# Kernel tuning notes

Hardware: AMD Instinct MI355X
Metric: run time of the kernel (lower is better)

The kernel has to match this reference:

```python
import jax, jax.numpy as jnp
import numpy as np

NUM_SLOTS = 8
SLOT_DIM = 3
WRITE_RATE = 0.1


def _amu(x, memory, Wk, bk, Ww, bw, Wg, bg, Wo, bo):
    """Associative Memory Unit.
    x: [B, T, Din], memory: [B, N, D] -> (outputs [B, T, Dout], memory [B, N, D]).
    Per step: softmax key-addressing read, gated erase/add write at WRITE_RATE,
    output = Linear(concat(x_t, read)).
    """
    xt = jnp.swapaxes(x, 0, 1)  # [T, B, Din]

    def step(mem, x_t):
        k = x_t @ Wk + bk                                   # [B, D]
        scores = jnp.einsum('bnd,bd->bn', mem, k)           # [B, N]
        w = jax.nn.softmax(scores, axis=-1)                 # addressing weights
        read = jnp.einsum('bn,bnd->bd', w, mem)             # [B, D]
        v = x_t @ Ww + bw                                   # write vector [B, D]
        e = jax.nn.sigmoid(x_t @ Wg + bg)                   # erase gate [B, D]
        we = w[:, :, None] * e[:, None, :]                  # [B, N, D]
        mem = mem * (1.0 - WRITE_RATE * we) + WRITE_RATE * w[:, :, None] * v[:, None, :]
        out = jnp.concatenate([x_t, read], axis=-1) @ Wo + bo
        return mem, out

    mem, outs = jax.lax.scan(step, memory, xt)
    return jnp.swapaxes(outs, 0, 1), mem


def setup_inputs() -> dict:
    key = jax.random.key(0)
    ks = jax.random.split(key, 12)
    B, T, D_in, D_hid, D_out = 64, 512, 128, 512, 128
    s = 0.05
    return {
        'inp': jax.random.normal(ks[0], (B, T, D_in), jnp.float32),
        'W1k': jax.random.normal(ks[1], (D_in, SLOT_DIM), jnp.float32) * s,
        'b1k': jnp.zeros((SLOT_DIM,), jnp.float32),
        'W1w': jax.random.normal(ks[2], (D_in, SLOT_DIM), jnp.float32) * s,
        'b1w': jnp.zeros((SLOT_DIM,), jnp.float32),
        'W1g': jax.random.normal(ks[3], (D_in, SLOT_DIM), jnp.float32) * s,
        'b1g': jnp.zeros((SLOT_DIM,), jnp.float32),
        'W1o': jax.random.normal(ks[4], (D_in + SLOT_DIM, D_hid), jnp.float32) * s,
        'b1o': jnp.zeros((D_hid,), jnp.float32),
        'W2k': jax.random.normal(ks[5], (D_hid, SLOT_DIM), jnp.float32) * s,
        'b2k': jnp.zeros((SLOT_DIM,), jnp.float32),
        'W2w': jax.random.normal(ks[6], (D_hid, SLOT_DIM), jnp.float32) * s,
        'b2w': jnp.zeros((SLOT_DIM,), jnp.float32),
        'W2g': jax.random.normal(ks[7], (D_hid, SLOT_DIM), jnp.float32) * s,
        'b2g': jnp.zeros((SLOT_DIM,), jnp.float32),
        'W2o': jax.random.normal(ks[8], (D_hid + SLOT_DIM, D_out), jnp.float32) * s,
        'b2o': jnp.zeros((D_out,), jnp.float32),
    }


def reference(inp, W1k, b1k, W1w, b1w, W1g, b1g, W1o, b1o,
              W2k, b2k, W2w, b2w, W2g, b2g, W2o, b2o):
    B = inp.shape[0]
    mem0 = jnp.zeros((B, NUM_SLOTS, SLOT_DIM), inp.dtype)
    o1, mem = _amu(inp, mem0, W1k, b1k, W1w, b1w, W1g, b1g, W1o, b1o)
    o1 = jax.nn.sigmoid(o1)  # self.layers = Sequential(Sigmoid())
    o2, mem = _amu(o1, mem, W2k, b2k, W2w, b2w, W2g, b2g, W2o, b2o)
    out = jax.nn.sigmoid(o2[:, -1, :])  # last timestep, then sigmoid
    return out
```

## Files before the change

kernel.cpp:

```cpp
#include <hip/hip_runtime.h>
#include <hip/hip_bf16.h>

#define B_ 64
#define T_ 512
#define LOG2E 1.4426950408889634f
#define PHASE_STEPS 16
#define NPHASE (T_/PHASE_STEPS)

typedef __attribute__((ext_vector_type(8))) short short8;
typedef __attribute__((ext_vector_type(4))) float f32x4;

__device__ __forceinline__ float fast_exp2(float x){ return __builtin_amdgcn_exp2f(x); }
__device__ __forceinline__ float fast_rcp(float x){ return __builtin_amdgcn_rcpf(x); }
__device__ __forceinline__ float sigmoidf_(float x){ return fast_rcp(1.0f + fast_exp2(-x*LOG2E)); }
__device__ __forceinline__ unsigned short f2bf(float f){
  union{float f; unsigned u;} v; v.f = f;
  unsigned r = v.u + 0x7fffu + ((v.u>>16)&1u);
  return (unsigned short)(r>>16);
}
__device__ __forceinline__ float bf2f(unsigned short u){
  union{unsigned u; float f;} v; v.u = ((unsigned)u)<<16; return v.f;
}

template<int CTRL>
__device__ __forceinline__ float dpp_xadd(float x){
  int y = __builtin_amdgcn_update_dpp(0, __float_as_int(x), CTRL, 0xf, 0xf, true);
  return x + __int_as_float(y);
}
__device__ __forceinline__ float dpp_sum8(float x){
  x = dpp_xadd<0xB1>(x);
  x = dpp_xadd<0x4E>(x);
  x = dpp_xadd<0x141>(x);
  return x;
}

__device__ __forceinline__ void lds_barrier(){
  asm volatile("s_waitcnt lgkmcnt(0)" ::: "memory");
  __builtin_amdgcn_s_barrier();
  asm volatile("" ::: "memory");
}

__global__ __launch_bounds__(256) void k_proj1(const float* __restrict__ X,
    const float* __restrict__ Wk, const float* __restrict__ bk,
    const float* __restrict__ Ww, const float* __restrict__ bw,
    const float* __restrict__ Wg, const float* __restrict__ bg,
    float* __restrict__ P1,
    const float* __restrict__ W1o,
    const float* __restrict__ W2k, const float* __restrict__ W2w, const float* __restrict__ W2g,
    unsigned short* __restrict__ W1oTb, unsigned short* __restrict__ W2cTb)
{
  __shared__ __align__(16) float A[64*132];
  __shared__ __align__(16) float WcT[9*132];
  __shared__ float bb[9];
  int tid = threadIdx.x;
  if (blockIdx.x >= 512){
    int idx = ((int)blockIdx.x - 512)*256 + tid;
    if (idx < 65536){
      int n = idx >> 7, k = idx & 127;
      W1oTb[idx] = f2bf(W1o[k*512 + n]);
    }
    if (idx < 8192){
      int j = idx >> 9, c = idx & 511;
      float v = 0.f;
      if (j < 3) v = W2k[c*3 + j];
      else if (j < 6) v = W2w[c*3 + j - 3];
      else if (j < 9) v = W2g[c*3 + j - 6];
      W2cTb[idx] = f2bf(v);
    }
    return;
  }
  long r0 = (long)blockIdx.x * 64;
  const float4* X4 = (const float4*)(X + r0*128);
  #pragma unroll
  for (int it=0; it<8; ++it){
    int f4 = tid + it*256;
    float4 v = X4[f4];
    int f = f4*4; int row = f>>7; int k = f&127;
    *(float4*)&A[row*132+k] = v;
  }
  #pragma unroll
  for (int it=0; it<5; ++it){
    int w0 = tid + it*256;
    if (w0 < 1152){
      int k = w0/9, j = w0%9;
      float val;
      if (j<3) val = Wk[k*3+j]; else if (j<6) val = Ww[k*3+j-3]; else val = Wg[k*3+j-6];
      WcT[j*132+k] = val;
    }
  }
  if (tid < 9){
    float v; if (tid<3) v = bk[tid]; else if (tid<6) v = bw[tid-3]; else v = bg[tid-6];
    bb[tid] = v;
  }
  __syncthreads();
  for (int o = tid; o < 576; o += 256){
    int row = o/9, j = o%9;
    const f32x4* Ar = (const f32x4*)(A + row*132);
    const f32x4* Wr = (const f32x4*)(WcT + j*132);
    f32x4 acc4 = {0.f,0.f,0.f,0.f};
    #pragma unroll
    for (int k4=0;k4<32;++k4){
      f32x4 a = Ar[k4], wv = Wr[k4];
      acc4[0]=fmaf(a[0],wv[0],acc4[0]);
      acc4[1]=fmaf(a[1],wv[1],acc4[1]);
      acc4[2]=fmaf(a[2],wv[2],acc4[2]);
      acc4[3]=fmaf(a[3],wv[3],acc4[3]);
    }
    float acc = bb[j] + (acc4[0]+acc4[1]) + (acc4[2]+acc4[3]);
    if (j<3) acc *= LOG2E;
    else if (j<6) acc *= 0.1f;
    else acc = 0.1f * sigmoidf_(acc);
    long r = r0 + row;
    int b = (int)(r >> 9); int t = (int)(r & 511);
    int bh = b >> 5, bl = b & 31;
    P1[(((long)bh*512 + t)*32 + bl)*12 + j] = acc;
  }
}

template<int STORE_SM>
__device__ __forceinline__ void scan_slim(const float* __restrict__ P,
                                          float* __restrict__ Out, int bh)
{
  __shared__ __align__(16) float buf[2][PHASE_STEPS*32*12];
  int tid = threadIdx.x;
  int wv = tid >> 6, lane = tid & 63;
  const float* Pb = P + (long)bh*512*384;
  if (wv == 8){
    #pragma unroll 1
    for (int p = 0; p < NPHASE; ++p){
      const float4* s4 = (const float4*)Pb + (long)p*1536;
      float4* d4 = (float4*)buf[p&1];
      #pragma unroll
      for (int c=0;c<2;++c){
        float4 tmp[12];
        #pragma unroll
        for (int i=0;i<12;++i) tmp[i] = s4[lane + (c*12+i)*64];
        #pragma unroll
        for (int i=0;i<12;++i) d4[lane + (c*12+i)*64] = tmp[i];
      }
      lds_barrier();
    }
    return;
  }
  if (lane >= 32) return;
  int g = lane >> 3, slot = lane & 7;
  int bl = wv*4 + g;
  int batch = bh*32 + bl;
  float* So = Out + ((long)batch*8 + slot)*4;
  float m0=0.f, m1=0.f, m2=0.f;
  f32x4 pfa[4], pfb[4]; float pfc[4];
  lds_barrier();
  #pragma unroll 1
  for (int p = 0; p < NPHASE; ++p){
    const float* bp = buf[p&1] + bl*12;
    const f32x4* bp4 = (const f32x4*)bp;
    #pragma unroll
    for (int u=0;u<3;++u){
      pfa[u]=bp4[u*96]; pfb[u]=bp4[u*96+1]; pfc[u]=bp[u*384+8];
    }
    #pragma unroll
    for (int s=0;s<PHASE_STEPS;++s){
      f32x4 A0=pfa[s&3], A1=pfb[s&3]; float e2=pfc[s&3];
      if (s+3 < PHASE_STEPS){
        int i3=(s+3)&3;
        pfa[i3]=bp4[(s+3)*96]; pfb[i3]=bp4[(s+3)*96+1]; pfc[i3]=bp[(s+3)*384+8];
      }
      float sc = fmaf(m2, A0[2], fmaf(m1, A0[1], m0*A0[0]));
      float pe = fast_exp2(sc);
      float S = dpp_sum8(pe);
      float rinv = fast_rcp(S);
      float w = pe * rinv;
      if (STORE_SM){
        f32x4 sv; sv[0]=pe; sv[1]=m0; sv[2]=m1; sv[3]=m2;
        *(f32x4*)(So + (long)(p*PHASE_STEPS+s)*2048) = sv;
      } else if (p == NPHASE-1 && s == PHASE_STEPS-1){
        float r0 = dpp_sum8(pe*m0);
        float r1 = dpp_sum8(pe*m1);
        float r2 = dpp_sum8(pe*m2);
        float rsel = (slot==0) ? r0 : ((slot==1) ? r1 : r2);
        rsel *= rinv;
        if (slot < 3) Out[slot*64 + batch] = rsel;
      }
      float v0=A0[3], v1=A1[0], v2=A1[1], e0=A1[2], e1=A1[3];
      m0 = fmaf(w, fmaf(-e0, m0, v0), m0);
      m1 = fmaf(w, fmaf(-e1, m1, v1), m1);
      m2 = fmaf(w, fmaf(-e2, m2, v2), m2);
    }
    if (p < NPHASE-1) lds_barrier();
  }
}

__global__ __launch_bounds__(576) void k_scan1(const float* __restrict__ P1,
                                               float* __restrict__ SM)
{
  scan_slim<1>(P1, SM, (int)blockIdx.x);
}

__global__ __launch_bounds__(576) void k_mega1(const float* __restrict__ P1,
    float* __restrict__ SM, const float* __restrict__ X,
    const unsigned short* __restrict__ W1oTb, const float* __restrict__ b1o,
    unsigned short* __restrict__ z1bf)
{
  if (blockIdx.x < 2){
    scan_slim<1>(P1, SM, (int)blockIdx.x);
    return;
  }
  int tid = threadIdx.x;
  if (tid >= 512) return;
  int w8 = tid >> 6, lane = tid & 63;
  int n16 = lane & 15, g4 = lane >> 4;
  long r0 = (long)(blockIdx.x - 2) * 16;

  short8 afr[4];
  const float* Xrow = X + (r0 + n16)*128;
  #pragma unroll
  for (int q=0;q<4;++q){
    f32x4 x0 = *(const f32x4*)(Xrow + q*32 + g4*8);
    f32x4 x1 = *(const f32x4*)(Xrow + q*32 + g4*8 + 4);
    short8 a;
    a[0]=(short)f2bf(x0[0]); a[1]=(short)f2bf(x0[1]);
    a[2]=(short)f2bf(x0[2]); a[3]=(short)f2bf(x0[3]);
    a[4]=(short)f2bf(x1[0]); a[5]=(short)f2bf(x1[1]);
    a[6]=(short)f2bf(x1[2]); a[7]=(short)f2bf(x1[3]);
    afr[q]=a;
  }
  #pragma unroll
  for (int tt=0; tt<4; ++tt){
    int gc = w8*64 + tt*16 + n16;
    f32x4 acc = {0.f,0.f,0.f,0.f};
    #pragma unroll
    for (int q=0;q<4;++q){
      short8 bf = *(const short8*)(W1oTb + gc*128 + q*32 + g4*8);
      acc = __builtin_amdgcn_mfma_f32_16x16x32_bf16(afr[q], bf, acc, 0,0,0);
    }
    float bias = b1o[gc];
    #pragma unroll
    for (int reg=0; reg<4; ++reg){
      int rowloc = g4*4 + reg;
      z1bf[(r0 + rowloc)*512 + gc] = f2bf(acc[reg] + bias);
    }
  }
}

__global__ __launch_bounds__(256) void k_fused2(
    const unsigned short* __restrict__ z1bf, const float* __restrict__ W1o,
    const float* __restrict__ SM, const unsigned short* __restrict__ W2cTb,
    const float* __restrict__ b2k, const float* __restrict__ b2w, const float* __restrict__ b2g,
    float* __restrict__ P2, float* __restrict__ O1last)
{
  __shared__ __align__(16) float rdS[48];
  __shared__ __align__(16) unsigned short o1b[16*520];
  __shared__ __align__(16) float pSum[4*16*16];
  int tid = threadIdx.x;
  long r0 = (long)blockIdx.x * 16;
  int b = (int)(r0 >> 9); int t0 = (int)(r0 & 511);

  if (tid < 128){
    int i = tid >> 3, slot = tid & 7;
    f32x4 v = *(const f32x4*)(SM + (((long)(t0+i)*64 + b)*8 + slot)*4);
    float S   = dpp_sum8(v[0]);
    float r0v = dpp_sum8(v[0]*v[1]);
    float r1v = dpp_sum8(v[0]*v[2]);
    float r2v = dpp_sum8(v[0]*v[3]);
    float rinv = fast_rcp(S);
    float rsel = (slot==0) ? r0v : ((slot==1) ? r1v : r2v);
    if (slot < 3) rdS[i*3+slot] = rsel*rinv;
  }
  __syncthreads();

  {
    int row = tid >> 4, seg = tid & 15, c0 = seg*32;
    float rd0v = rdS[row*3+0], rd1v = rdS[row*3+1], rd2v = rdS[row*3+2];
    const unsigned short* zr = z1bf + (r0 + row)*512 + c0;
    bool last = (t0 == 496) && (row == 15);
    #pragma unroll
    for (int ch=0; ch<4; ++ch){
      short8 z8 = *(const short8*)(zr + ch*8);
      int cc = c0 + ch*8;
      f32x4 wa0 = *(const f32x4*)(W1o + 128*512 + cc);
      f32x4 wa1 = *(const f32x4*)(W1o + 128*512 + cc + 4);
      f32x4 wb0 = *(const f32x4*)(W1o + 129*512 + cc);
      f32x4 wb1 = *(const f32x4*)(W1o + 129*512 + cc + 4);
      f32x4 wc0 = *(const f32x4*)(W1o + 130*512 + cc);
      f32x4 wc1 = *(const f32x4*)(W1o + 130*512 + cc + 4);
      #pragma unroll
      for (int j=0;j<8;++j){
        float z = bf2f((unsigned short)z8[j]);
        float w0 = (j<4)? wa0[j&3] : wa1[j&3];
        float w1 = (j<4)? wb0[j&3] : wb1[j&3];
        float w2 = (j<4)? wc0[j&3] : wc1[j&3];
        float o1 = sigmoidf_(z + rd0v*w0 + rd1v*w1 + rd2v*w2);
        o1b[row*520 + cc + j] = f2bf(o1);
        if (last) O1last[b*512 + cc + j] = o1;
      }
    }
  }
  __syncthreads();

  int w = tid >> 6, lane = tid & 63;
  int n16 = lane & 15, g4 = lane >> 4;
  f32x4 accP = {0.f,0.f,0.f,0.f};
  #pragma unroll
  for (int q2=0; q2<4; ++q2){
    int kk = w*128 + q2*32;
    short8 a2 = *(const short8*)(o1b + n16*520 + kk + g4*8);
    short8 bb2 = *(const short8*)(W2cTb + n16*512 + kk + g4*8);
    accP = __builtin_amdgcn_mfma_f32_16x16x32_bf16(a2, bb2, accP, 0,0,0);
  }
  #pragma unroll
  for (int reg=0;reg<4;++reg){
    int rowloc = g4*4+reg;
    pSum[w*256 + rowloc*16 + n16] = accP[reg];
  }
  __syncthreads();
  if (tid < 144){
    int r = tid/9, j = tid%9;
    float s = pSum[r*16+j] + pSum[256+r*16+j] + pSum[512+r*16+j] + pSum[768+r*16+j];
    float outv;
    if (j<3){ s += b2k[j]; outv = s*LOG2E; }
    else if (j<6){ s += b2w[j-3]; outv = 0.1f*s; }
    else { s += b2g[j-6]; outv = 0.1f*sigmoidf_(s); }
    int t = t0 + r;
    int bh = b >> 5, bl = b & 31;
    P2[(((long)bh*512 + t)*32 + bl)*12 + j] = outv;
  }
}

__global__ __launch_bounds__(256) void k_fused(const float* __restrict__ X,
    const float* __restrict__ W1o, const float* __restrict__ b1o,
    const float* __restrict__ SM,
    const unsigned short* __restrict__ W1oTb, const unsigned short* __restrict__ W2cTb,
    const float* __restrict__ b2k, const float* __restrict__ b2w, const float* __restrict__ b2g,
    float* __restrict__ P2, float* __restrict__ O1last)
{
  __shared__ __align__(16) float rdS[48];
  __shared__ __align__(16) unsigned short o1b[16*520];
  __shared__ __align__(16) float pSum[4*16*16];
  int tid = threadIdx.x;
  int w = tid >> 6, lane = tid & 63;
  int n16 = lane & 15, g4 = lane >> 4;
  long r0 = (long)blockIdx.x * 16;
  int b = (int)(r0 >> 9); int t0 = (int)(r0 & 511);

  if (tid < 128){
    int i = tid >> 3, slot = tid & 7;
    f32x4 v = *(const f32x4*)(SM + (((long)(t0+i)*64 + b)*8 + slot)*4);
    float S   = dpp_sum8(v[0]);
    float r0v = dpp_sum8(v[0]*v[1]);
    float r1v = dpp_sum8(v[0]*v[2]);
    float r2v = dpp_sum8(v[0]*v[3]);
    float rinv = fast_rcp(S);
    float rsel = (slot==0) ? r0v : ((slot==1) ? r1v : r2v);
    if (slot < 3) rdS[i*3+slot] = rsel*rinv;
  }

  short8 afr[4];
  const float* Xrow = X + (r0 + n16)*128;
  #pragma unroll
  for (int q=0;q<4;++q){
    f32x4 x0 = *(const f32x4*)(Xrow + q*32 + g4*8);
    f32x4 x1 = *(const f32x4*)(Xrow + q*32 + g4*8 + 4);
    short8 a;
    a[0]=(short)f2bf(x0[0]); a[1]=(short)f2bf(x0[1]);
    a[2]=(short)f2bf(x0[2]); a[3]=(short)f2bf(x0[3]);
    a[4]=(short)f2bf(x1[0]); a[5]=(short)f2bf(x1[1]);
    a[6]=(short)f2bf(x1[2]); a[7]=(short)f2bf(x1[3]);
    afr[q]=a;
  }
  __syncthreads();

  f32x4 ra = *(const f32x4*)(rdS + g4*12);
  f32x4 rb = *(const f32x4*)(rdS + g4*12 + 4);
  f32x4 rc = *(const f32x4*)(rdS + g4*12 + 8);
  float rd0[4] = { ra[0], ra[3], rb[2], rc[1] };
  float rd1[4] = { ra[1], rb[0], rb[3], rc[2] };
  float rd2[4] = { ra[2], rb[1], rc[0], rc[3] };

  #pragma unroll
  for (int tt=0; tt<8; ++tt){
    int gc = w*128 + tt*16 + n16;
    f32x4 acc = {0.f,0.f,0.f,0.f};
    #pragma unroll
    for (int q=0;q<4;++q){
      short8 bf = *(const short8*)(W1oTb + gc*128 + q*32 + g4*8);
      acc = __builtin_amdgcn_mfma_f32_16x16x32_bf16(afr[q], bf, acc, 0,0,0);
    }
    float bias = b1o[gc];
    float wr0 = W1o[128*512+gc], wr1 = W1o[129*512+gc], wr2 = W1o[130*512+gc];
    #pragma unroll
    for (int reg=0; reg<4; ++reg){
      int rowloc = g4*4 + reg;
      float z = acc[reg] + bias + rd0[reg]*wr0 + rd1[reg]*wr1 + rd2[reg]*wr2;
      float o1 = sigmoidf_(z);
      o1b[rowloc*520 + gc] = f2bf(o1);
      if (t0 == 496 && rowloc == 15) O1last[b*512 + gc] = o1;
    }
  }

  f32x4 accP = {0.f,0.f,0.f,0.f};
  #pragma unroll
  for (int q2=0; q2<4; ++q2){
    int kk = w*128 + q2*32;
    short8 a2 = *(const short8*)(o1b + n16*520 + kk + g4*8);
    short8 bb2 = *(const short8*)(W2cTb + n16*512 + kk + g4*8);
    accP = __builtin_amdgcn_mfma_f32_16x16x32_bf16(a2, bb2, accP, 0,0,0);
  }
  #pragma unroll
  for (int reg=0;reg<4;++reg){
    int rowloc = g4*4+reg;
    pSum[w*256 + rowloc*16 + n16] = accP[reg];
  }
  __syncthreads();
  if (tid < 144){
    int r = tid/9, j = tid%9;
    float s = pSum[r*16+j] + pSum[256+r*16+j] + pSum[512+r*16+j] + pSum[768+r*16+j];
    float outv;
    if (j<3){ s += b2k[j]; outv = s*LOG2E; }
    else if (j<6){ s += b2w[j-3]; outv = 0.1f*s; }
    else { s += b2g[j-6]; outv = 0.1f*sigmoidf_(s); }
    int t = t0 + r;
    int bh = b >> 5, bl = b & 31;
    P2[(((long)bh*512 + t)*32 + bl)*12 + j] = outv;
  }
}

__global__ __launch_bounds__(576) void k_scan2_opart(const float* __restrict__ P2,
    float* __restrict__ R2F,
    const float* __restrict__ O1last, const float* __restrict__ W2o,
    const float* __restrict__ b2o, float* __restrict__ Opart)
{
  if (blockIdx.x < 2){
    scan_slim<0>(P2, R2F, (int)blockIdx.x);
    return;
  }
  __shared__ __align__(16) float s2[512];
  int b = blockIdx.x - 2; int tid = threadIdx.x;
  if (tid < 128)
    ((float4*)s2)[tid] = ((const float4*)(O1last + b*512))[tid];
  __syncthreads();
  if (tid < 128){
    float acc = b2o[tid];
    #pragma unroll 8
    for (int n=0;n<512;++n) acc = fmaf(s2[n], W2o[n*128+tid], acc);
    Opart[b*128+tid] = acc;
  }
}

__global__ __launch_bounds__(256) void k_final(const float* __restrict__ Opart,
    const float* __restrict__ R2F, const float* __restrict__ W2o,
    float* __restrict__ out)
{
  int idx = blockIdx.x*256 + threadIdx.x;
  if (idx < 8192){
    int b = idx >> 7; int o = idx & 127;
    float r0 = R2F[b], r1 = R2F[64+b], r2 = R2F[128+b];
    float v = Opart[idx]
            + r0*W2o[512*128+o] + r1*W2o[513*128+o] + r2*W2o[514*128+o];
    out[idx] = sigmoidf_(v);
  }
}

extern "C" void kernel_launch(void* const* d_in, const int* in_sizes, int n_in,
                              void* d_out, int out_size, void* d_ws, size_t ws_size,
                              hipStream_t stream)
{
  const float* X  = (const float*)d_in[0];
  const float* W1k= (const float*)d_in[1]; const float* b1k=(const float*)d_in[2];
  const float* W1w= (const float*)d_in[3]; const float* b1w=(const float*)d_in[4];
  const float* W1g= (const float*)d_in[5]; const float* b1g=(const float*)d_in[6];
  const float* W1o= (const float*)d_in[7]; const float* b1o=(const float*)d_in[8];
  const float* W2k= (const float*)d_in[9]; const float* b2k=(const float*)d_in[10];
  const float* W2w= (const float*)d_in[11]; const float* b2w=(const float*)d_in[12];
  const float* W2g= (const float*)d_in[13]; const float* b2g=(const float*)d_in[14];
  const float* W2o= (const float*)d_in[15]; const float* b2o=(const float*)d_in[16];

  float* ws = (float*)d_ws;
  float* P1     = ws;
  float* SM     = P1 + 393216;
  float* O1last = SM + 1048576;
  float* R2F    = O1last + 32768;
  float* Opart  = R2F + 192;
  unsigned short* W1oTb = (unsigned short*)(Opart + 8192);
  unsigned short* W2cTb = W1oTb + 65536;
  unsigned short* z1bf  = W2cTb + 8192;
  float* P2     = P1;
  float* out    = (float*)d_out;

  bool bigws = ws_size >= (size_t)39633664ull;

  hipLaunchKernelGGL(k_proj1, dim3(768), dim3(256), 0, stream,
                     X, W1k,b1k, W1w,b1w, W1g,b1g, P1,
                     W1o, W2k, W2w, W2g, W1oTb, W2cTb);
  if (bigws){
    hipLaunchKernelGGL(k_mega1, dim3(2050), dim3(576), 0, stream,
                       P1, SM, X, W1oTb, b1o, z1bf);
    hipLaunchKernelGGL(k_fused2, dim3(2048), dim3(256), 0, stream,
                       z1bf, W1o, SM, W2cTb, b2k, b2w, b2g, P2, O1last);
  } else {
    hipLaunchKernelGGL(k_scan1, dim3(2), dim3(576), 0, stream, P1, SM);
    hipLaunchKernelGGL(k_fused, dim3(2048), dim3(256), 0, stream,
                       X, W1o, b1o, SM, W1oTb, W2cTb, b2k, b2w, b2g, P2, O1last);
  }
  hipLaunchKernelGGL(k_scan2_opart, dim3(66), dim3(576), 0, stream,
                     P2, R2F, O1last, W2o, b2o, Opart);
  hipLaunchKernelGGL(k_final, dim3(32), dim3(256), 0, stream,
                     Opart, R2F, W2o, out);
}
```

Before: 252.7 us.

## Fuse final projection into second scan and move Opart GEMV into fused2

On the big-workspace path, the last-timestep output projection (O1last @ W2o) is computed inside k_fused2 by the block that owns t=496..511, using the bf16 o1 row already staged in shared memory. The second scan kernel then applies the read-vector correction and the final sigmoid itself, which removes the separate k_scan2_opart GEMV blocks and the k_final launch. It also raises scan wave priority with s_setprio and adds launch_bounds min-blocks hints. The trade-off is a small precision change, since o1 now comes from bf16 instead of fp32, plus a serial 512-length GEMV loop in one fused2 block.

Result: slower. 273.0 us (+8.0%).

```diff
diff --git a/kernel.cpp b/kernel.cpp
--- a/kernel.cpp
+++ b/kernel.cpp
@@ -117,13 +117,18 @@
   }
 }
 
-template<int STORE_SM>
+template<int MODE>
 __device__ __forceinline__ void scan_slim(const float* __restrict__ P,
-                                          float* __restrict__ Out, int bh)
+                                          float* __restrict__ Out, int bh,
+                                          const float* __restrict__ Opart,
+                                          const float* __restrict__ W2o,
+                                          float* __restrict__ outp)
 {
   __shared__ __align__(16) float buf[2][PHASE_STEPS*32*12];
+  __shared__ float rS[32][4];
   int tid = threadIdx.x;
   int wv = tid >> 6, lane = tid & 63;
+  __builtin_amdgcn_s_setprio(1);
   const float* Pb = P + (long)bh*512*384;
   if (wv == 8){
     #pragma unroll 1
@@ -140,69 +145,82 @@
       }
       lds_barrier();
     }
-    return;
-  }
-  if (lane >= 32) return;
-  int g = lane >> 3, slot = lane & 7;
-  int bl = wv*4 + g;
-  int batch = bh*32 + bl;
-  float* So = Out + ((long)batch*8 + slot)*4;
-  float m0=0.f, m1=0.f, m2=0.f;
-  f32x4 pfa[4], pfb[4]; float pfc[4];
-  lds_barrier();
-  #pragma unroll 1
-  for (int p = 0; p < NPHASE; ++p){
-    const float* bp = buf[p&1] + bl*12;
-    const f32x4* bp4 = (const f32x4*)bp;
-    #pragma unroll
-    for (int u=0;u<3;++u){
-      pfa[u]=bp4[u*96]; pfb[u]=bp4[u*96+1]; pfc[u]=bp[u*384+8];
-    }
-    #pragma unroll
-    for (int s=0;s<PHASE_STEPS;++s){
-      f32x4 A0=pfa[s&3], A1=pfb[s&3]; float e2=pfc[s&3];
-      if (s+3 < PHASE_STEPS){
-        int i3=(s+3)&3;
-        pfa[i3]=bp4[(s+3)*96]; pfb[i3]=bp4[(s+3)*96+1]; pfc[i3]=bp[(s+3)*384+8];
+  } else if (lane < 32){
+    int g = lane >> 3, slot = lane & 7;
+    int bl = wv*4 + g;
+    int batch = bh*32 + bl;
+    float* So = Out + ((long)batch*8 + slot)*4;
+    float m0=0.f, m1=0.f, m2=0.f;
+    f32x4 pfa[4], pfb[4]; float pfc[4];
+    lds_barrier();
+    #pragma unroll 1
+    for (int p = 0; p < NPHASE; ++p){
+      const float* bp = buf[p&1] + bl*12;
+      const f32x4* bp4 = (const f32x4*)bp;
+      #pragma unroll
+      for (int u=0;u<3;++u){
+        pfa[u]=bp4[u*96]; pfb[u]=bp4[u*96+1]; pfc[u]=bp[u*384+8];
       }
-      float sc = fmaf(m2, A0[2], fmaf(m1, A0[1], m0*A0[0]));
-      float pe = fast_exp2(sc);
-      float S = dpp_sum8(pe);
-      float rinv = fast_rcp(S);
-      float w = pe * rinv;
-      if (STORE_SM){
-        f32x4 sv; sv[0]=pe; sv[1]=m0; sv[2]=m1; sv[3]=m2;
-        *(f32x4*)(So + (long)(p*PHASE_STEPS+s)*2048) = sv;
-      } else if (p == NPHASE-1 && s == PHASE_STEPS-1){
-        float r0 = dpp_sum8(pe*m0);
-        float r1 = dpp_sum8(pe*m1);
-        float r2 = dpp_sum8(pe*m2);
-        float rsel = (slot==0) ? r0 : ((slot==1) ? r1 : r2);
-        rsel *= rinv;
-        if (slot < 3) Out[slot*64 + batch] = rsel;
+      #pragma unroll
+      for (int s=0;s<PHASE_STEPS;++s){
+        f32x4 A0=pfa[s&3], A1=pfb[s&3]; float e2=pfc[s&3];
+        if (s+3 < PHASE_STEPS){
+          int i3=(s+3)&3;
+          pfa[i3]=bp4[(s+3)*96]; pfb[i3]=bp4[(s+3)*96+1]; pfc[i3]=bp[(s+3)*384+8];
+        }
+        float sc = fmaf(m2, A0[2], fmaf(m1, A0[1], m0*A0[0]));
+        float pe = fast_exp2(sc);
+        float S = dpp_sum8(pe);
+        float rinv = fast_rcp(S);
+        float w = pe * rinv;
+        if (MODE == 1){
+          f32x4 sv; sv[0]=pe; sv[1]=m0; sv[2]=m1; sv[3]=m2;
+          *(f32x4*)(So + (long)(p*PHASE_STEPS+s)*2048) = sv;
+        } else if (p == NPHASE-1 && s == PHASE_STEPS-1){
+          float r0 = dpp_sum8(pe*m0);
+          float r1 = dpp_sum8(pe*m1);
+          float r2 = dpp_sum8(pe*m2);
+          float rsel = (slot==0) ? r0 : ((slot==1) ? r1 : r2);
+          rsel *= rinv;
+          if (MODE == 0){ if (slot < 3) Out[slot*64 + batch] = rsel; }
+          else          { if (slot < 3) rS[bl][slot] = rsel; }
+        }
+        float v0=A0[3], v1=A1[0], v2=A1[1], e0=A1[2], e1=A1[3];
+        m0 = fmaf(w, fmaf(-e0, m0, v0), m0);
+        m1 = fmaf(w, fmaf(-e1, m1, v1), m1);
+        m2 = fmaf(w, fmaf(-e2, m2, v2), m2);
       }
-      float v0=A0[3], v1=A1[0], v2=A1[1], e0=A1[2], e1=A1[3];
-      m0 = fmaf(w, fmaf(-e0, m0, v0), m0);
-      m1 = fmaf(w, fmaf(-e1, m1, v1), m1);
-      m2 = fmaf(w, fmaf(-e2, m2, v2), m2);
-    }
-    if (p < NPHASE-1) lds_barrier();
-  }
-}
-
-__global__ __launch_bounds__(576) void k_scan1(const float* __restrict__ P1,
-                                               float* __restrict__ SM)
-{
-  scan_slim<1>(P1, SM, (int)blockIdx.x);
-}
-
-__global__ __launch_bounds__(576) void k_mega1(const float* __restrict__ P1,
+      if (p < NPHASE-1) lds_barrier();
+    }
+  }
+  if constexpr (MODE == 2){
+    lds_barrier();
+    __builtin_amdgcn_s_setprio(0);
+    for (int idx = tid; idx < 4096; idx += 576){
+      int bl = idx >> 7, o = idx & 127;
+      int batch = bh*32 + bl;
+      float v = Opart[batch*128 + o]
+              + rS[bl][0]*W2o[512*128+o]
+              + rS[bl][1]*W2o[513*128+o]
+              + rS[bl][2]*W2o[514*128+o];
+      outp[batch*128 + o] = sigmoidf_(v);
+    }
+  }
+}
+
+__global__ __launch_bounds__(576, 1) void k_scan1(const float* __restrict__ P1,
+                                                  float* __restrict__ SM)
+{
+  scan_slim<1>(P1, SM, (int)blockIdx.x, nullptr, nullptr, nullptr);
+}
+
+__global__ __launch_bounds__(576, 1) void k_mega1(const float* __restrict__ P1,
     float* __restrict__ SM, const float* __restrict__ X,
     const unsigned short* __restrict__ W1oTb, const float* __restrict__ b1o,
     unsigned short* __restrict__ z1bf)
 {
   if (blockIdx.x < 2){
-    scan_slim<1>(P1, SM, (int)blockIdx.x);
+    scan_slim<1>(P1, SM, (int)blockIdx.x, nullptr, nullptr, nullptr);
     return;
   }
   int tid = threadIdx.x;
@@ -246,7 +264,8 @@
     const unsigned short* __restrict__ z1bf, const float* __restrict__ W1o,
     const float* __restrict__ SM, const unsigned short* __restrict__ W2cTb,
     const float* __restrict__ b2k, const float* __restrict__ b2w, const float* __restrict__ b2g,
-    float* __restrict__ P2, float* __restrict__ O1last)
+    const float* __restrict__ W2o, const float* __restrict__ b2o,
+    float* __restrict__ P2, float* __restrict__ Opart)
 {
   __shared__ __align__(16) float rdS[48];
   __shared__ __align__(16) unsigned short o1b[16*520];
@@ -272,7 +291,6 @@
     int row = tid >> 4, seg = tid & 15, c0 = seg*32;
     float rd0v = rdS[row*3+0], rd1v = rdS[row*3+1], rd2v = rdS[row*3+2];
     const unsigned short* zr = z1bf + (r0 + row)*512 + c0;
-    bool last = (t0 == 496) && (row == 15);
     #pragma unroll
     for (int ch=0; ch<4; ++ch){
       short8 z8 = *(const short8*)(zr + ch*8);
@@ -291,11 +309,18 @@
         float w2 = (j<4)? wc0[j&3] : wc1[j&3];
         float o1 = sigmoidf_(z + rd0v*w0 + rd1v*w1 + rd2v*w2);
         o1b[row*520 + cc + j] = f2bf(o1);
-        if (last) O1last[b*512 + cc + j] = o1;
       }
     }
   }
   __syncthreads();
+
+  if (t0 == 496 && tid < 128){
+    float acc = b2o[tid];
+    #pragma unroll 8
+    for (int n=0;n<512;++n)
+      acc = fmaf(bf2f(o1b[15*520+n]), W2o[n*128+tid], acc);
+    Opart[b*128+tid] = acc;
+  }
 
   int w = tid >> 6, lane = tid & 63;
   int n16 = lane & 15, g4 = lane >> 4;
@@ -326,6 +351,13 @@
   }
 }
 
+__global__ __launch_bounds__(576, 1) void k_scan2f(const float* __restrict__ P2,
+    const float* __restrict__ Opart, const float* __restrict__ W2o,
+    float* __restrict__ outp)
+{
+  scan_slim<2>(P2, nullptr, (int)blockIdx.x, Opart, W2o, outp);
+}
+
 __global__ __launch_bounds__(256) void k_fused(const float* __restrict__ X,
     const float* __restrict__ W1o, const float* __restrict__ b1o,
     const float* __restrict__ SM,
@@ -424,13 +456,13 @@
   }
 }
 
-__global__ __launch_bounds__(576) void k_scan2_opart(const float* __restrict__ P2,
+__global__ __launch_bounds__(576, 1) void k_scan2_opart(const float* __restrict__ P2,
     float* __restrict__ R2F,
     const float* __restrict__ O1last, const float* __restrict__ W2o,
     const float* __restrict__ b2o, float* __restrict__ Opart)
 {
   if (blockIdx.x < 2){
-    scan_slim<0>(P2, R2F, (int)blockIdx.x);
+    scan_slim<0>(P2, R2F, (int)blockIdx.x, nullptr, nullptr, nullptr);
     return;
   }
   __shared__ __align__(16) float s2[512];
@@ -495,14 +527,16 @@
     hipLaunchKernelGGL(k_mega1, dim3(2050), dim3(576), 0, stream,
                        P1, SM, X, W1oTb, b1o, z1bf);
     hipLaunchKernelGGL(k_fused2, dim3(2048), dim3(256), 0, stream,
-                       z1bf, W1o, SM, W2cTb, b2k, b2w, b2g, P2, O1last);
+                       z1bf, W1o, SM, W2cTb, b2k, b2w, b2g, W2o, b2o, P2, Opart);
+    hipLaunchKernelGGL(k_scan2f, dim3(2), dim3(576), 0, stream,
+                       P2, Opart, W2o, out);
   } else {
     hipLaunchKernelGGL(k_scan1, dim3(2), dim3(576), 0, stream, P1, SM);
     hipLaunchKernelGGL(k_fused, dim3(2048), dim3(256), 0, stream,
                        X, W1o, b1o, SM, W1oTb, W2cTb, b2k, b2w, b2g, P2, O1last);
-  }
-  hipLaunchKernelGGL(k_scan2_opart, dim3(66), dim3(576), 0, stream,
-                     P2, R2F, O1last, W2o, b2o, Opart);
-  hipLaunchKernelGGL(k_final, dim3(32), dim3(256), 0, stream,
-                     Opart, R2F, W2o, out);
-}
+    hipLaunchKernelGGL(k_scan2_opart, dim3(66), dim3(576), 0, stream,
+                       P2, R2F, O1last, W2o, b2o, Opart);
+    hipLaunchKernelGGL(k_final, dim3(32), dim3(256), 0, stream,
+                       Opart, R2F, W2o, out);
+  }
+}
```
